# Kernel optimization log

Measured on AMD Instinct MI355X. Metric: run time of the kernel, lower is better.

Reference implementation:

```python
import jax, jax.numpy as jnp
import numpy as np

NLAT, NLON = 64, 64
CIN = 512
HEADS = 8


def _cc_weights(n):
    # Clenshaw-Curtis quadrature weights on [-1, 1] for nodes cos(k*pi/(n-1)),
    # as used by torch-harmonics for the 'equiangular' grid. Weights sum to 2.
    N = n - 1
    theta = np.pi * np.arange(n) / N
    m = N // 2
    j = np.arange(1, m + 1)
    b = np.where(2 * j == N, 1.0, 2.0)
    S = (b / (4.0 * j ** 2 - 1.0))[None, :] * np.cos(2.0 * j[None, :] * theta[:, None])
    w = 1.0 - S.sum(axis=1)
    c = np.full(n, 2.0)
    c[0] = 1.0
    c[-1] = 1.0
    return c * w / N


def _log_quad_weights(nlat, nlon):
    # _precompute_latitudes flips nodes/weights; then 2*pi*w/nlon tiled over lon.
    w = _cc_weights(nlat)[::-1].copy()
    qw = 2.0 * np.pi * w / nlon                       # (nlat,)
    qw = np.tile(qw[:, None], (1, nlon)).reshape(-1)  # (nlat*nlon,)
    return jnp.asarray(np.log(qw), dtype=jnp.float32)


def setup_inputs() -> dict:
    key = jax.random.key(0)
    ks = jax.random.split(key, 5)
    s_qkv = float(np.sqrt(3.0 / CIN))   # scale for q/k/v 1x1-conv weights
    s_proj = float(np.sqrt(3.0 / CIN))  # out_channels == CIN
    u = lambda k, sh, s: jax.random.uniform(k, sh, jnp.float32, -s, s)
    return dict(
        query=jax.random.normal(ks[0], (1, CIN, NLAT, NLON), jnp.float32),
        q_w=u(ks[1], (CIN, CIN), s_qkv), q_b=jnp.zeros((CIN,), jnp.float32),
        k_w=u(ks[2], (CIN, CIN), s_qkv), k_b=jnp.zeros((CIN,), jnp.float32),
        v_w=u(ks[3], (CIN, CIN), s_qkv), v_b=jnp.zeros((CIN,), jnp.float32),
        p_w=u(ks[4], (CIN, CIN), s_proj), p_b=jnp.zeros((CIN,), jnp.float32),
        log_quad_weights=_log_quad_weights(NLAT, NLON),
    )


def reference(query, q_w, q_b, k_w, k_b, v_w, v_b, p_w, p_b, log_quad_weights):
    B, C, H, W = query.shape
    hd = C // HEADS  # head dim (k_channels == out_channels == in_channels)

    def proj_tokens(x, w, b):
        # 1x1 conv == channel matmul, then split heads and flatten H*W tokens
        y = jnp.einsum('bihw,oi->bohw', x, w) + b[None, :, None, None]
        return y.reshape(B, HEADS, -1, H, W).transpose(0, 1, 3, 4, 2).reshape(B, HEADS, H * W, -1)

    q = proj_tokens(query, q_w, q_b)  # (B, heads, HW, hd)
    k = proj_tokens(query, k_w, k_b)  # self-attention: key/value default to query
    v = proj_tokens(query, v_w, v_b)

    scale = 1.0 / jnp.sqrt(jnp.asarray(hd, dtype=q.dtype))
    # additive log-quadrature bias over keys (broadcast over batch/head/query)
    logits = jnp.einsum('bhqd,bhkd->bhqk', q, k) * scale + log_quad_weights[None, None, None, :]
    attn = jax.nn.softmax(logits, axis=-1)
    out = jnp.einsum('bhqk,bhkd->bhqd', attn, v)          # (B, heads, HW, hd)
    out = out.transpose(0, 1, 3, 2).reshape(B, HEADS * hd, H, W)
    return jnp.einsum('bihw,oi->bohw', out, p_w) + p_b[None, :, None, None]
```

## Files before the change

### kernel.cpp

```cpp
#include <hip/hip_runtime.h>

typedef unsigned short u16;
typedef unsigned int u32;
typedef __bf16 bf16x8 __attribute__((ext_vector_type(8)));
typedef float f32x4 __attribute__((ext_vector_type(4)));
typedef unsigned short u16x4 __attribute__((ext_vector_type(4)));

#define LOG2E 1.4426950408889634f

#if __has_builtin(__builtin_amdgcn_exp2f)
#define EXP2F(x) __builtin_amdgcn_exp2f(x)
#else
#define EXP2F(x) exp2f(x)
#endif

__device__ __forceinline__ u16 f2bf(float f) {
    union { float f; u32 u; } a; a.f = f;
    u32 u = a.u;
    u += 0x7FFFu + ((u >> 16) & 1u);
    return (u16)(u >> 16);
}
__device__ __forceinline__ bf16x8 ldg8(const u16* p) {
    return *reinterpret_cast<const bf16x8*>(p);
}
#if __has_builtin(__builtin_amdgcn_cvt_pk_bf16_f32)
__device__ __forceinline__ u32 pack2(float a, float b) {
    auto r = __builtin_amdgcn_cvt_pk_bf16_f32(a, b);
    return __builtin_bit_cast(u32, r);
}
#else
__device__ __forceinline__ u32 pack2(float a, float b) {
    u32 ua = __float_as_uint(a) + 0x8000u;
    u32 ub = __float_as_uint(b) + 0x8000u;
    return __builtin_amdgcn_perm(ub, ua, 0x07060302);
}
#endif
__device__ __forceinline__ void async16(const void* g, void* l) {
    __builtin_amdgcn_global_load_lds(
        (const __attribute__((address_space(1))) u32*)g,
        (__attribute__((address_space(3))) u32*)l, 16, 0, 0);
}

#define MFMA16(a, b, c) __builtin_amdgcn_mfma_f32_16x16x32_bf16((a), (b), (c), 0, 0, 0)

__global__ __launch_bounds__(256) void prep(const float* __restrict__ X,
                                            u16* __restrict__ Xt,
                                            const float* __restrict__ s0,
                                            const float* __restrict__ s1,
                                            const float* __restrict__ s2,
                                            const float* __restrict__ s3,
                                            u16* __restrict__ Wqkv,
                                            u16* __restrict__ Wp,
                                            const float* __restrict__ lqw,
                                            float* __restrict__ lqw2g) {
    __shared__ u16 tile[64][65];
    const int tid = threadIdx.x;
    const int y = blockIdx.y;

    if (y < 8) {
        const int t0 = blockIdx.x * 64;
        const int c0 = y * 64;
#pragma unroll
        for (int i = 0; i < 16; ++i) {
            int idx = tid + i * 256;
            int r = idx >> 6, cc = idx & 63;
            tile[r][cc] = f2bf(X[(size_t)(c0 + r) * 4096 + t0 + cc]);
        }
        __syncthreads();
#pragma unroll
        for (int i = 0; i < 16; ++i) {
            int idx = tid + i * 256;
            int tr = idx >> 6, cc = idx & 63;
            Xt[(size_t)(t0 + tr) * 512 + c0 + cc] = tile[cc][tr];
        }
    } else if (y < 12) {
        const int m = y - 8;
        const float* s = (m == 0) ? s0 : (m == 1) ? s1 : (m == 2) ? s2 : s3;
        u16* d = (m == 3) ? Wp : Wqkv + (size_t)m * 262144;
#pragma unroll
        for (int j = 0; j < 4; ++j) {
            int i = blockIdx.x * 1024 + j * 256 + tid;
            float4 v = reinterpret_cast<const float4*>(s)[i];
            u16x4 o;
            o[0] = f2bf(v.x); o[1] = f2bf(v.y); o[2] = f2bf(v.z); o[3] = f2bf(v.w);
            reinterpret_cast<u16x4*>(d)[i] = o;
        }
    } else {
        if (blockIdx.x < 4) {
            int i = blockIdx.x * 256 + tid;
            float4 v = reinterpret_cast<const float4*>(lqw)[i];
            v.x *= LOG2E; v.y *= LOG2E; v.z *= LOG2E; v.w *= LOG2E;
            reinterpret_cast<float4*>(lqw2g)[i] = v;
        }
    }
}

__global__ __launch_bounds__(512, 2) void qkv_gemm(const u16* __restrict__ Wqkv,
                                                   const u16* __restrict__ Xt,
                                                   const float* __restrict__ qb,
                                                   const float* __restrict__ kb,
                                                   const float* __restrict__ vb,
                                                   u16* __restrict__ Qt,
                                                   u16* __restrict__ Kt,
                                                   u16* __restrict__ Vp) {
    __shared__ __align__(16) u16 Al[2][128 * 32];
    __shared__ __align__(16) u16 Bl[2][128 * 32];

    const int tid = threadIdx.x;
    const int w = tid >> 6, lane = tid & 63;
    const int quad = lane >> 4, lm = lane & 15;
    const int wm = w & 1, wn = w >> 1;
    const int n0 = blockIdx.x * 128;
    const int my = blockIdx.y;
    const int m0 = my * 128;

    const int arow = lane >> 2;
    const int sch = (lane & 3) ^ ((lane >> 3) & 3);
    const u16* agp = Wqkv + (size_t)(m0 + w * 16 + arow) * 512 + sch * 8;
    const u16* bgp = Xt + (size_t)(n0 + w * 16 + arow) * 512 + sch * 8;

    async16(agp, &Al[0][w * 16 * 32]);
    async16(bgp, &Bl[0][w * 16 * 32]);
    agp += 32; bgp += 32;

    const int FOFF = lm * 64 + ((quad ^ ((lm >> 1) & 3)) << 4);

    f32x4 acc[4][2];
#pragma unroll
    for (int mt = 0; mt < 4; ++mt)
#pragma unroll
        for (int bt = 0; bt < 2; ++bt) acc[mt][bt] = (f32x4){0.f, 0.f, 0.f, 0.f};

    __syncthreads();

    for (int s = 0; s < 16; ++s) {
        const int buf = s & 1;
        if (s < 15) {
            async16(agp, &Al[buf ^ 1][w * 16 * 32]);
            async16(bgp, &Bl[buf ^ 1][w * 16 * 32]);
            agp += 32; bgp += 32;
        }
        const char* Ab = (const char*)&Al[buf][0];
        const char* Bb = (const char*)&Bl[buf][0];
        bf16x8 af[4], bfr[2];
#pragma unroll
        for (int mt = 0; mt < 4; ++mt)
            af[mt] = *(const bf16x8*)(Ab + wm * 4096 + mt * 1024 + FOFF);
#pragma unroll
        for (int bt = 0; bt < 2; ++bt)
            bfr[bt] = *(const bf16x8*)(Bb + wn * 2048 + bt * 1024 + FOFF);
#pragma unroll
        for (int mt = 0; mt < 4; ++mt)
#pragma unroll
            for (int bt = 0; bt < 2; ++bt)
                acc[mt][bt] = MFMA16(af[mt], bfr[bt], acc[mt][bt]);
        __syncthreads();
    }

    const int mat = my >> 2;
    const float* bias = (mat == 0) ? qb : (mat == 1) ? kb : vb;
    const int chbase = (my & 3) * 128 + wm * 64 + quad * 4;

    if (mat < 2) {
        u16* out = mat ? Kt : Qt;
        const float sc = mat ? 1.0f : 0.125f * LOG2E;
#pragma unroll
        for (int mt = 0; mt < 4; ++mt) {
            const int ch = chbase + mt * 16;
            float4 bv = *(const float4*)(bias + ch);
            float bvf[4] = {bv.x, bv.y, bv.z, bv.w};
#pragma unroll
            for (int bt = 0; bt < 2; ++bt) {
                int tok = n0 + wn * 32 + bt * 16 + lm;
                u16x4 pk;
#pragma unroll
                for (int r = 0; r < 4; ++r)
                    pk[r] = f2bf((acc[mt][bt][r] + bvf[r]) * sc);
                *(u16x4*)(out + (size_t)tok * 512 + ch) = pk;
            }
        }
    } else {
#pragma unroll
        for (int mt = 0; mt < 4; ++mt) {
            const int ch = chbase + mt * 16;
            float4 bv = *(const float4*)(bias + ch);
            float bvf[4] = {bv.x, bv.y, bv.z, bv.w};
#pragma unroll
            for (int bt = 0; bt < 2; ++bt) {
                int g = bt * 16 + lm;
                int col = n0 + wn * 32 + 8 * ((g >> 2) & 3) + 4 * ((g >> 4) & 1) + (g & 3);
#pragma unroll
                for (int r = 0; r < 4; ++r)
                    Vp[(size_t)(ch + r) * 4096 + col] = f2bf(acc[mt][bt][r] + bvf[r]);
            }
        }
    }
}

__global__ __launch_bounds__(256, 2) void out_gemm(const u16* __restrict__ Wp,
                                                   const u16* __restrict__ Ot,
                                                   const float* __restrict__ pb,
                                                   float* __restrict__ out) {
    __shared__ __align__(16) u16 Al[2][128 * 32];
    __shared__ __align__(16) u16 Bl[2][64 * 32];

    const int tid = threadIdx.x;
    const int w = tid >> 6, lane = tid & 63;
    const int quad = lane >> 4, lm = lane & 15;
    const int wm = w & 1, wn = w >> 1;
    const int n0 = blockIdx.x * 64;
    const int m0 = blockIdx.y * 128;

    const int arow = lane >> 2;
    const int sch = (lane & 3) ^ ((lane >> 3) & 3);
    const u16* agp0 = Wp + (size_t)(m0 + w * 16 + arow) * 512 + sch * 8;
    const u16* agp1 = agp0 + (size_t)64 * 512;
    const u16* bgp = Ot + (size_t)(n0 + w * 16 + arow) * 512 + sch * 8;

    async16(agp0, &Al[0][w * 16 * 32]);
    async16(agp1, &Al[0][(64 + w * 16) * 32]);
    async16(bgp, &Bl[0][w * 16 * 32]);
    agp0 += 32; agp1 += 32; bgp += 32;

    const int FOFF = lm * 64 + ((quad ^ ((lm >> 1) & 3)) << 4);

    f32x4 acc[4][2];
#pragma unroll
    for (int mt = 0; mt < 4; ++mt)
#pragma unroll
        for (int bt = 0; bt < 2; ++bt) acc[mt][bt] = (f32x4){0.f, 0.f, 0.f, 0.f};

    __syncthreads();

    for (int s = 0; s < 16; ++s) {
        const int buf = s & 1;
        if (s < 15) {
            async16(agp0, &Al[buf ^ 1][w * 16 * 32]);
            async16(agp1, &Al[buf ^ 1][(64 + w * 16) * 32]);
            async16(bgp, &Bl[buf ^ 1][w * 16 * 32]);
            agp0 += 32; agp1 += 32; bgp += 32;
        }
        const char* Ab = (const char*)&Al[buf][0];
        const char* Bb = (const char*)&Bl[buf][0];
        bf16x8 af[4], bfr[2];
#pragma unroll
        for (int mt = 0; mt < 4; ++mt)
            af[mt] = *(const bf16x8*)(Ab + wm * 4096 + mt * 1024 + FOFF);
#pragma unroll
        for (int bt = 0; bt < 2; ++bt)
            bfr[bt] = *(const bf16x8*)(Bb + wn * 2048 + bt * 1024 + FOFF);
#pragma unroll
        for (int mt = 0; mt < 4; ++mt)
#pragma unroll
            for (int bt = 0; bt < 2; ++bt)
                acc[mt][bt] = MFMA16(af[mt], bfr[bt], acc[mt][bt]);
        __syncthreads();
    }

#pragma unroll
    for (int mt = 0; mt < 4; ++mt) {
        const int ch = m0 + wm * 64 + mt * 16 + quad * 4;
        float4 bv = *(const float4*)(pb + ch);
        float bvf[4] = {bv.x, bv.y, bv.z, bv.w};
#pragma unroll
        for (int bt = 0; bt < 2; ++bt) {
            int tok = n0 + wn * 32 + bt * 16 + lm;
#pragma unroll
            for (int r = 0; r < 4; ++r)
                out[(size_t)(ch + r) * 4096 + tok] = acc[mt][bt][r] + bvf[r];
        }
    }
}

#define WAITVM(N) asm volatile("s_waitcnt vmcnt(" #N ")" ::: "memory")

__global__ __launch_bounds__(256, 2) void flash_attn(const u16* __restrict__ Qt,
                                                     const u16* __restrict__ Kt,
                                                     const u16* __restrict__ Vp,
                                                     const float* __restrict__ lqw2g,
                                                     u16* __restrict__ Ot) {
    __shared__ __align__(16) char smem[65536];

    const int tid = threadIdx.x;
    const int w = tid >> 6, lane = tid & 63;
    const int quad = lane >> 4, lm = lane & 15;
    const int bid = blockIdx.x;
    const int h = bid & 7, hq = h * 64;
    const int q0 = (bid >> 3) * 64;
    const int kstart = w * 1024;

    char* kvw = smem + w * 16384;

    const int srow = lane >> 3;
    const int schunk = (lane & 7) ^ srow;
    const u16* kg = Kt + (size_t)(kstart + srow) * 512 + hq + schunk * 8;
    const u16* vg = Vp + (size_t)(hq + 2 * srow + (schunk >> 2)) * 4096 +
                    kstart + (schunk & 3) * 8;

    bf16x8 bq0[4], bq1[4];
#pragma unroll
    for (int s = 0; s < 4; ++s) {
        const u16* qb = Qt + (size_t)(q0 + s * 16 + lm) * 512 + hq + quad * 8;
        bq0[s] = ldg8(qb);
        bq1[s] = ldg8(qb + 32);
    }

    f32x4 breg0 = *(const f32x4*)(lqw2g + kstart + quad * 4);
    f32x4 breg1 = *(const f32x4*)(lqw2g + kstart + 16 + quad * 4);
    const float* bptr = lqw2g + kstart + 32 + quad * 4;

    const int A0 = lm * 128 + ((quad ^ (lm & 7)) << 4);
    const int A1 = A0 ^ 64;
    const int AV = (lm >> 1) * 128 +
                   (((4 * (lm & 1) + quad) ^ ((lm >> 1) & 7)) << 4);

#define STAGEBLK(DST)                                                          \
    {                                                                          \
        char* nb = (DST);                                                      \
        async16(kg, nb);                                                       \
        async16(kg + 8 * 512, nb + 1024);                                      \
        async16(kg + 16 * 512, nb + 2048);                                     \
        async16(kg + 24 * 512, nb + 3072);                                     \
        async16(vg, nb + 4096);                                                \
        async16(vg + (size_t)16 * 4096, nb + 5120);                            \
        async16(vg + (size_t)32 * 4096, nb + 6144);                            \
        async16(vg + (size_t)48 * 4096, nb + 7168);                            \
        kg += 32 * 512; vg += 32;                                              \
    }

    STAGEBLK(kvw)
    STAGEBLK(kvw + 8192)

    union { u32 u[4]; bf16x8 v; } onesu;
    onesu.u[0] = onesu.u[1] = onesu.u[2] = onesu.u[3] = 0x3F803F80u;
    const bf16x8 onesv = onesu.v;

    f32x4 acc_o[4][4];
#pragma unroll
    for (int mt = 0; mt < 4; ++mt)
#pragma unroll
        for (int s = 0; s < 4; ++s) acc_o[mt][s] = (f32x4){0.f, 0.f, 0.f, 0.f};
    f32x4 acc_l[4];
#pragma unroll
    for (int s = 0; s < 4; ++s) acc_l[s] = (f32x4){0.f, 0.f, 0.f, 0.f};

    union { u32 u[4]; bf16x8 v; } pb_[4];
    bf16x8 pv0, pv1, pv2, pv3;
    int bufsel = 0;

#define BODY(WN, DOBIAS, DOSTAGE, DOPV)                                        \
    {                                                                          \
        WAITVM(WN);                                                            \
        const char* Kb = kvw + bufsel;                                         \
        const char* Vb = Kb + 4096;                                            \
        bf16x8 k00 = *(const bf16x8*)(Kb + A0);                                \
        bf16x8 k01 = *(const bf16x8*)(Kb + A1);                                \
        bf16x8 k10 = *(const bf16x8*)(Kb + 2048 + A0);                         \
        bf16x8 k11 = *(const bf16x8*)(Kb + 2048 + A1);                         \
        bf16x8 nv0 = *(const bf16x8*)(Vb + AV);                                \
        bf16x8 nv1 = *(const bf16x8*)(Vb + 1024 + AV);                         \
        bf16x8 nv2 = *(const bf16x8*)(Vb + 2048 + AV);                         \
        bf16x8 nv3 = *(const bf16x8*)(Vb + 3072 + AV);                         \
        if (DOPV) {                                                            \
            _Pragma("unroll")                                                  \
            for (int s = 0; s < 4; ++s) {                                      \
                acc_o[0][s] = MFMA16(pv0, pb_[s].v, acc_o[0][s]);              \
                acc_o[1][s] = MFMA16(pv1, pb_[s].v, acc_o[1][s]);              \
                acc_o[2][s] = MFMA16(pv2, pb_[s].v, acc_o[2][s]);              \
                acc_o[3][s] = MFMA16(pv3, pb_[s].v, acc_o[3][s]);              \
                acc_l[s] = MFMA16(onesv, pb_[s].v, acc_l[s]);                  \
            }                                                                  \
        }                                                                      \
        _Pragma("unroll")                                                      \
        for (int s = 0; s < 4; ++s) {                                          \
            f32x4 a = MFMA16(k00, bq0[s], breg0);                              \
            a = MFMA16(k01, bq1[s], a);                                        \
            pb_[s].u[0] = pack2(EXP2F(a[0]), EXP2F(a[1]));                     \
            pb_[s].u[1] = pack2(EXP2F(a[2]), EXP2F(a[3]));                     \
        }                                                                      \
        _Pragma("unroll")                                                      \
        for (int s = 0; s < 4; ++s) {                                          \
            f32x4 c = MFMA16(k10, bq0[s], breg1);                              \
            c = MFMA16(k11, bq1[s], c);                                        \
            pb_[s].u[2] = pack2(EXP2F(c[0]), EXP2F(c[1]));                     \
            pb_[s].u[3] = pack2(EXP2F(c[2]), EXP2F(c[3]));                     \
        }                                                                      \
        if (DOBIAS) {                                                          \
            breg0 = *(const f32x4*)(bptr);                                     \
            breg1 = *(const f32x4*)(bptr + 16);                                \
            bptr += 32;                                                        \
        }                                                                      \
        pv0 = nv0; pv1 = nv1; pv2 = nv2; pv3 = nv3;                            \
        if (DOSTAGE) STAGEBLK(kvw + bufsel)                                    \
        bufsel ^= 8192;                                                        \
    }

    BODY(8, true, true, false)
    for (int t = 1; t < 30; ++t)
        BODY(10, true, true, true)
    BODY(10, true, false, true)
    BODY(2, false, false, true)

#undef BODY
#undef STAGEBLK

#pragma unroll
    for (int s = 0; s < 4; ++s) {
        acc_o[0][s] = MFMA16(pv0, pb_[s].v, acc_o[0][s]);
        acc_o[1][s] = MFMA16(pv1, pb_[s].v, acc_o[1][s]);
        acc_o[2][s] = MFMA16(pv2, pb_[s].v, acc_o[2][s]);
        acc_o[3][s] = MFMA16(pv3, pb_[s].v, acc_o[3][s]);
        acc_l[s] = MFMA16(onesv, pb_[s].v, acc_l[s]);
    }

    __syncthreads();
    float* mbuf = (float*)smem;
    if (w != 0) {
        float* ob = mbuf + (w - 1) * 4096;
#pragma unroll
        for (int s = 0; s < 4; ++s) {
            const int r = s * 16 + lm;
#pragma unroll
            for (int mt = 0; mt < 4; ++mt) {
                const int sl = (mt * 4 + quad) ^ lm;
                *(f32x4*)(ob + r * 64 + sl * 4) = acc_o[mt][s];
            }
        }
        if (quad == 0) {
#pragma unroll
            for (int s = 0; s < 4; ++s)
                mbuf[12288 + (w - 1) * 64 + s * 16 + lm] = acc_l[s][0];
        }
    }
    __syncthreads();
    if (w != 0) return;

#pragma unroll
    for (int s = 0; s < 4; ++s) {
        const int r = s * 16 + lm;
        float lsum = acc_l[s][0];
#pragma unroll
        for (int p = 0; p < 3; ++p)
            lsum += mbuf[12288 + p * 64 + r];
        const float inv = 1.0f / lsum;
#pragma unroll
        for (int mt = 0; mt < 4; ++mt) {
            const int sl = (mt * 4 + quad) ^ lm;
            f32x4 o = acc_o[mt][s];
#pragma unroll
            for (int p = 0; p < 3; ++p)
                o += *(const f32x4*)(mbuf + p * 4096 + r * 64 + sl * 4);
            u16x4 pkv;
#pragma unroll
            for (int r2 = 0; r2 < 4; ++r2)
                pkv[r2] = f2bf(o[r2] * inv);
            *reinterpret_cast<u16x4*>(Ot + (size_t)(q0 + r) * 512 +
                                      hq + mt * 16 + quad * 4) = pkv;
        }
    }
}

extern "C" void kernel_launch(void* const* d_in, const int* in_sizes, int n_in,
                              void* d_out, int out_size, void* d_ws, size_t ws_size,
                              hipStream_t stream) {
    (void)in_sizes; (void)n_in; (void)out_size; (void)ws_size;
    const float* X   = (const float*)d_in[0];
    const float* qw  = (const float*)d_in[1];
    const float* qb  = (const float*)d_in[2];
    const float* kw  = (const float*)d_in[3];
    const float* kb  = (const float*)d_in[4];
    const float* vw  = (const float*)d_in[5];
    const float* vb  = (const float*)d_in[6];
    const float* pw  = (const float*)d_in[7];
    const float* pb  = (const float*)d_in[8];
    const float* lqw = (const float*)d_in[9];

    const size_t E = (size_t)4096 * 512;
    const size_t WE = (size_t)512 * 512;
    u16* Xt    = (u16*)d_ws;
    u16* Qt    = Xt + E;
    u16* Kt    = Qt + E;
    u16* Vp    = Kt + E;
    u16* Wqkv  = Vp + E;
    u16* Wp    = Wqkv + 3 * WE;
    float* lqw2g = (float*)(Wp + WE);
    u16* Ot    = Xt;

    prep<<<dim3(64, 13), dim3(256), 0, stream>>>(X, Xt, qw, kw, vw, pw,
                                                 Wqkv, Wp, lqw, lqw2g);
    qkv_gemm<<<dim3(32, 12), dim3(512), 0, stream>>>(Wqkv, Xt, qb, kb, vb, Qt, Kt, Vp);
    flash_attn<<<dim3(512), dim3(256), 0, stream>>>(Qt, Kt, Vp, lqw2g, Ot);
    out_gemm<<<dim3(64, 4), dim3(256), 0, stream>>>(Wp, Ot, pb, (float*)d_out);
}
```

Baseline: 77.75 us.

## Pre-swizzle K/V into contiguous per-head tiles and raise MFMA wave priority

The QKV GEMM epilogue now writes K and V directly into a combined buffer laid out as contiguous 8 KB per-head, per-32-key tiles, already in the XOR-swizzled shared-memory order. The flash-attention kernel can then stage each tile with fully contiguous 16-byte async loads at lane*8 offsets, where before it did strided gathers across Kt and Vp. This is meant to cut address arithmetic and uncoalesced global traffic in the attention inner loop. It also wraps the MFMA/exp section in s_setprio(1) to favour compute waves. The V epilogue stores become scattered 2-byte writes, which may make the GEMM slower.

```diff
diff --git a/kernel.cpp b/kernel.cpp
--- a/kernel.cpp
+++ b/kernel.cpp
@@ -101,8 +101,7 @@
                                                    const float* __restrict__ kb,
                                                    const float* __restrict__ vb,
                                                    u16* __restrict__ Qt,
-                                                   u16* __restrict__ Kt,
-                                                   u16* __restrict__ Vp) {
+                                                   u16* __restrict__ KV) {
     __shared__ __align__(16) u16 Al[2][128 * 32];
     __shared__ __align__(16) u16 Bl[2][128 * 32];
 
@@ -161,9 +160,8 @@
     const float* bias = (mat == 0) ? qb : (mat == 1) ? kb : vb;
     const int chbase = (my & 3) * 128 + wm * 64 + quad * 4;
 
-    if (mat < 2) {
-        u16* out = mat ? Kt : Qt;
-        const float sc = mat ? 1.0f : 0.125f * LOG2E;
+    if (mat == 0) {
+        const float sc = 0.125f * LOG2E;
 #pragma unroll
         for (int mt = 0; mt < 4; ++mt) {
             const int ch = chbase + mt * 16;
@@ -176,22 +174,53 @@
 #pragma unroll
                 for (int r = 0; r < 4; ++r)
                     pk[r] = f2bf((acc[mt][bt][r] + bvf[r]) * sc);
-                *(u16x4*)(out + (size_t)tok * 512 + ch) = pk;
+                *(u16x4*)(Qt + (size_t)tok * 512 + ch) = pk;
             }
         }
-    } else {
+    } else if (mat == 1) {
 #pragma unroll
         for (int mt = 0; mt < 4; ++mt) {
             const int ch = chbase + mt * 16;
             float4 bv = *(const float4*)(bias + ch);
             float bvf[4] = {bv.x, bv.y, bv.z, bv.w};
+            const int hh = ch >> 6;
+            const int D0 = ch & 63;
+            const int cp = D0 >> 3;
+            const int e0 = D0 & 7;
+#pragma unroll
+            for (int bt = 0; bt < 2; ++bt) {
+                int tok = n0 + wn * 32 + bt * 16 + lm;
+                int t = tok >> 5, key = tok & 31;
+                int c = cp ^ (key & 7);
+                u16x4 pk;
+#pragma unroll
+                for (int r = 0; r < 4; ++r)
+                    pk[r] = f2bf(acc[mt][bt][r] + bvf[r]);
+                *(u16x4*)(KV + (size_t)(hh * 128 + t) * 4096 + key * 64 + c * 8 + e0) = pk;
+            }
+        }
+    } else {
+#pragma unroll
+        for (int mt = 0; mt < 4; ++mt) {
+            const int ch = chbase + mt * 16;
+            float4 bv = *(const float4*)(bias + ch);
+            float bvf[4] = {bv.x, bv.y, bv.z, bv.w};
+            const int hh = ch >> 6;
+            const int D0 = ch & 63;
 #pragma unroll
             for (int bt = 0; bt < 2; ++bt) {
                 int g = bt * 16 + lm;
-                int col = n0 + wn * 32 + 8 * ((g >> 2) & 3) + 4 * ((g >> 4) & 1) + (g & 3);
-#pragma unroll
-                for (int r = 0; r < 4; ++r)
-                    Vp[(size_t)(ch + r) * 4096 + col] = f2bf(acc[mt][bt][r] + bvf[r]);
+                int key2 = 8 * ((g >> 2) & 3) + 4 * ((g >> 4) & 1) + (g & 3);
+                int t = (n0 >> 5) + wn;
+                int kc = key2 >> 3, ke = key2 & 7;
+                u16* vdst = KV + (size_t)(hh * 128 + t) * 4096 + 2048 + ke;
+#pragma unroll
+                for (int r = 0; r < 4; ++r) {
+                    int D = D0 + r;
+                    int rl = (D >> 4) * 8 + ((D >> 1) & 7);
+                    int c = ((D >> 1) & 7) ^ (4 * (D & 1) + kc);
+                    vdst[rl * 64 + c * 8] = f2bf(acc[mt][bt][r] + bvf[r]);
+                }
             }
         }
     }
@@ -275,8 +304,7 @@
 #define WAITVM(N) asm volatile("s_waitcnt vmcnt(" #N ")" ::: "memory")
 
 __global__ __launch_bounds__(256, 2) void flash_attn(const u16* __restrict__ Qt,
-                                                     const u16* __restrict__ Kt,
-                                                     const u16* __restrict__ Vp,
+                                                     const u16* __restrict__ KV,
                                                      const float* __restrict__ lqw2g,
                                                      u16* __restrict__ Ot) {
     __shared__ __align__(16) char smem[65536];
@@ -291,11 +319,7 @@
 
     char* kvw = smem + w * 16384;
 
-    const int srow = lane >> 3;
-    const int schunk = (lane & 7) ^ srow;
-    const u16* kg = Kt + (size_t)(kstart + srow) * 512 + hq + schunk * 8;
-    const u16* vg = Vp + (size_t)(hq + 2 * srow + (schunk >> 2)) * 4096 +
-                    kstart + (schunk & 3) * 8;
+    const u16* kvs = KV + ((size_t)(h * 128 + w * 32) * 4096) + (size_t)lane * 8;
 
     bf16x8 bq0[4], bq1[4];
 #pragma unroll
@@ -317,15 +341,15 @@
 #define STAGEBLK(DST)                                                          \
     {                                                                          \
         char* nb = (DST);                                                      \
-        async16(kg, nb);                                                       \
-        async16(kg + 8 * 512, nb + 1024);                                      \
-        async16(kg + 16 * 512, nb + 2048);                                     \
-        async16(kg + 24 * 512, nb + 3072);                                     \
-        async16(vg, nb + 4096);                                                \
-        async16(vg + (size_t)16 * 4096, nb + 5120);                            \
-        async16(vg + (size_t)32 * 4096, nb + 6144);                            \
-        async16(vg + (size_t)48 * 4096, nb + 7168);                            \
-        kg += 32 * 512; vg += 32;                                              \
+        async16(kvs, nb);                                                      \
+        async16(kvs + 512, nb + 1024);                                         \
+        async16(kvs + 1024, nb + 2048);                                        \
+        async16(kvs + 1536, nb + 3072);                                        \
+        async16(kvs + 2048, nb + 4096);                                        \
+        async16(kvs + 2560, nb + 5120);                                        \
+        async16(kvs + 3072, nb + 6144);                                        \
+        async16(kvs + 3584, nb + 7168);                                        \
+        kvs += 4096;                                                           \
     }
 
     STAGEBLK(kvw)
@@ -361,6 +385,7 @@
         bf16x8 nv1 = *(const bf16x8*)(Vb + 1024 + AV);                         \
         bf16x8 nv2 = *(const bf16x8*)(Vb + 2048 + AV);                         \
         bf16x8 nv3 = *(const bf16x8*)(Vb + 3072 + AV);                         \
+        __builtin_amdgcn_s_setprio(1);                                         \
         if (DOPV) {                                                            \
             _Pragma("unroll")                                                  \
             for (int s = 0; s < 4; ++s) {                                      \
@@ -385,6 +410,7 @@
             pb_[s].u[2] = pack2(EXP2F(c[0]), EXP2F(c[1]));                     \
             pb_[s].u[3] = pack2(EXP2F(c[2]), EXP2F(c[3]));                     \
         }                                                                      \
+        __builtin_amdgcn_s_setprio(0);                                         \
         if (DOBIAS) {                                                          \
             breg0 = *(const f32x4*)(bptr);                                     \
             breg1 = *(const f32x4*)(bptr + 16);                                \
@@ -479,16 +505,15 @@
     const size_t WE = (size_t)512 * 512;
     u16* Xt    = (u16*)d_ws;
     u16* Qt    = Xt + E;
-    u16* Kt    = Qt + E;
-    u16* Vp    = Kt + E;
-    u16* Wqkv  = Vp + E;
+    u16* KV    = Qt + E;
+    u16* Wqkv  = KV + 2 * E;
     u16* Wp    = Wqkv + 3 * WE;
     float* lqw2g = (float*)(Wp + WE);
     u16* Ot    = Xt;
 
     prep<<<dim3(64, 13), dim3(256), 0, stream>>>(X, Xt, qw, kw, vw, pw,
                                                  Wqkv, Wp, lqw, lqw2g);
-    qkv_gemm<<<dim3(32, 12), dim3(512), 0, stream>>>(Wqkv, Xt, qb, kb, vb, Qt, Kt, Vp);
-    flash_attn<<<dim3(512), dim3(256), 0, stream>>>(Qt, Kt, Vp, lqw2g, Ot);
+    qkv_gemm<<<dim3(32, 12), dim3(512), 0, stream>>>(Wqkv, Xt, qb, kb, vb, Qt, KV);
+    flash_attn<<<dim3(512), dim3(256), 0, stream>>>(Qt, KV, lqw2g, Ot);
     out_gemm<<<dim3(64, 4), dim3(256), 0, stream>>>(Wp, Ot, pb, (float*)d_out);
 }
```

After: 77.35 us. No clear change (-0.5%).
